# Kernel optimization log

Hardware: AMD Instinct MI355X
Metric: run time of the kernel (lower is better)

## Reference

```python
import jax, jax.numpy as jnp
import numpy as np

NUM_HEADS = 16

def _w8a8_linear(x_q, x_scale, w_q, w_scale, bias):
    # W8A8 GEMM with dynamic per-token input scale and per-output-channel weight scale
    # x_q: [N, Din] int8 values, w_q: [Dout, Din] int8 values
    acc = jnp.matmul(x_q.astype(jnp.float32), w_q.astype(jnp.float32).T)  # [N, Dout]
    return acc * (x_scale[:, None] * w_scale[None, :]) + bias[None, :]


def setup_inputs() -> dict:
    key = jax.random.key(0)
    ks = jax.random.split(key, 16)
    B, S, D = 2, 2048, 1024
    N = B * S
    def int8(k, shape):
        return jax.random.randint(k, shape, -127, 128, dtype=jnp.int32)
    inp = {
        "x_q": int8(ks[0], (N, D)),
        "x_scale": jax.random.uniform(ks[1], (N,), jnp.float32, 0.005, 0.02),
        "wq": int8(ks[2], (D, D)),
        "wq_scale": jax.random.uniform(ks[3], (D,), jnp.float32, 0.005, 0.02),
        "bq": jax.random.normal(ks[4], (D,), jnp.float32) * 0.02,
        "wk": int8(ks[5], (D, D)),
        "wk_scale": jax.random.uniform(ks[6], (D,), jnp.float32, 0.005, 0.02),
        "bk": jax.random.normal(ks[7], (D,), jnp.float32) * 0.02,
        "wv": int8(ks[8], (D, D)),
        "wv_scale": jax.random.uniform(ks[9], (D,), jnp.float32, 0.005, 0.02),
        "bv": jax.random.normal(ks[10], (D,), jnp.float32) * 0.02,
        "wo": int8(ks[11], (D, D)),
        "wo_scale": jax.random.uniform(ks[12], (D,), jnp.float32, 0.005, 0.02),
        "bo": jax.random.normal(ks[13], (D,), jnp.float32) * 0.02,
        "bsz": B,
        "qlen": S,
    }
    return inp


def reference(x_q, x_scale, wq, wq_scale, bq, wk, wk_scale, bk,
              wv, wv_scale, bv, wo, wo_scale, bo, bsz, qlen):
    D = wq.shape[0]
    hd = D // NUM_HEADS
    # quantized QKV projections (dequant fused into GEMM epilogue)
    q = _w8a8_linear(x_q, x_scale, wq, wq_scale, bq).reshape(bsz, qlen, NUM_HEADS, hd)
    k = _w8a8_linear(x_q, x_scale, wk, wk_scale, bk).reshape(bsz, qlen, NUM_HEADS, hd)
    v = _w8a8_linear(x_q, x_scale, wv, wv_scale, bv).reshape(bsz, qlen, NUM_HEADS, hd)
    # flash_attn_func(softmax_scale=None, causal=False) => scale = 1/sqrt(head_dim)
    scale = 1.0 / jnp.sqrt(jnp.float32(hd))
    scores = jnp.einsum('bqhd,bkhd->bhqk', q, k) * scale
    probs = jax.nn.softmax(scores, axis=-1)
    attn = jnp.einsum('bhqk,bkhd->bqhd', probs, v).reshape(bsz * qlen, D)
    # invoke_quant: dynamic per-token symmetric int8 quantization of attn output
    o_scale = jnp.max(jnp.abs(attn), axis=-1) / 127.0  # [N]
    o_q = jnp.clip(jnp.round(attn / o_scale[:, None]), -127.0, 127.0)
    # quantized out projection
    out = _w8a8_linear(o_q, o_scale, wo, wo_scale, bo)  # [N, D]
    return out
```

## Files before the change

kernel.cpp:

```cpp
#include <hip/hip_runtime.h>

#define D_MODEL 1024
#define NTOK    4096
#define SEQ     2048
#define NH      16
#define HD      64

typedef __bf16 bh8  __attribute__((ext_vector_type(8)));
typedef __bf16 bf4  __attribute__((ext_vector_type(4)));
typedef float  f32x4 __attribute__((ext_vector_type(4)));
typedef int    i32x4 __attribute__((ext_vector_type(4)));

__device__ __forceinline__ unsigned short f2bf(float f) {
  unsigned int u = __float_as_uint(f);
  u += 0x7fffu + ((u >> 16) & 1u);
  return (unsigned short)(u >> 16);
}
__device__ __forceinline__ float bf2f(unsigned short h) {
  return __uint_as_float(((unsigned int)h) << 16);
}
__device__ __forceinline__ float exp2a(float x) {
  float r; asm("v_exp_f32 %0, %1" : "=v"(r) : "v"(x)); return r;
}
__device__ __forceinline__ void gl16(const void* g, void* l) {
  __builtin_amdgcn_global_load_lds((const __attribute__((address_space(1))) unsigned int*)g,
                                   (__attribute__((address_space(3))) unsigned int*)l, 16, 0, 0);
}

__device__ __forceinline__ void pack_row(const int* src, unsigned* dst, int m, int t) {
  int4 w = *(const int4*)(src + (size_t)m * 1024 + t * 4);
  unsigned p01 = __builtin_amdgcn_perm((unsigned)w.y, (unsigned)w.x, 0x00000400u);
  unsigned p23 = __builtin_amdgcn_perm((unsigned)w.w, (unsigned)w.z, 0x00000400u);
  unsigned r   = __builtin_amdgcn_perm(p23, p01, 0x05040100u);
  int kg = t >> 4, c = (t >> 2) & 3, b4 = t & 3, sw = (m >> 1) & 3;
  dst[(size_t)m * 256 + kg * 16 + ((c ^ sw) << 2) + b4] = r;
}
__launch_bounds__(256)
__global__ void pack_x_k(const int* __restrict__ src, unsigned* __restrict__ dst) {
  pack_row(src, dst, blockIdx.x, threadIdx.x);
}
__launch_bounds__(256)
__global__ void pack_w_k(const int* __restrict__ s0, const int* __restrict__ s1,
                         const int* __restrict__ s2, const int* __restrict__ s3,
                         unsigned* __restrict__ d0, unsigned* __restrict__ d1,
                         unsigned* __restrict__ d2, unsigned* __restrict__ d3) {
  int wsel = blockIdx.x >> 10, m = blockIdx.x & 1023;
  const int* src = wsel == 0 ? s0 : wsel == 1 ? s1 : wsel == 2 ? s2 : s3;
  unsigned*  dst = wsel == 0 ? d0 : wsel == 1 ? d1 : wsel == 2 ? d2 : d3;
  pack_row(src, dst, m, threadIdx.x);
}

__launch_bounds__(256, 2)
__global__ void gemmQKV_k(const signed char* __restrict__ xp,
                          const signed char* __restrict__ wqp,
                          const signed char* __restrict__ wkp,
                          const signed char* __restrict__ wvp,
                          const float* __restrict__ xs,
                          const float* __restrict__ wqs, const float* __restrict__ bq,
                          const float* __restrict__ wks, const float* __restrict__ bk,
                          const float* __restrict__ wvs, const float* __restrict__ bv,
                          float SC,
                          unsigned short* __restrict__ qhi, unsigned short* __restrict__ qlo,
                          unsigned short* __restrict__ khi, unsigned short* __restrict__ klo,
                          unsigned short* __restrict__ vtw)
{
  __shared__ __align__(16) signed char As[2][8192];
  __shared__ __align__(16) signed char Bs[2][8192];
  const int id = blockIdx.x, z = id >> 8, rb = id & 255;
  const int t = threadIdx.x, wid = t >> 6, lane = t & 63, g = lane >> 4, li = lane & 15;
  const int wm = wid >> 1, wn = wid & 1;
  const signed char *Ap, *Bp;
  int m0, n0;
  if (z == 2) { Ap = wvp; Bp = xp; m0 = (rb & 7) * 128; n0 = (rb >> 3) * 128; }
  else        { Ap = xp; Bp = z ? wkp : wqp; m0 = (rb >> 3) * 128; n0 = (rb & 7) * 128; }

  i32x4 acc[4][4];
#pragma unroll
  for (int i = 0; i < 4; ++i)
#pragma unroll
    for (int j = 0; j < 4; ++j) acc[i][j] = (i32x4){0, 0, 0, 0};

  const int unitBase = wid * 2;
#pragma unroll
  for (int i = 0; i < 2; ++i) {
    int unit = (unitBase + i) * 64 + lane, r = unit >> 2, c = unit & 3;
    gl16(Ap + (size_t)(m0 + r) * 1024 + c * 16, (char*)As[0] + (unitBase + i) * 1024);
    gl16(Bp + (size_t)(n0 + r) * 1024 + c * 16, (char*)Bs[0] + (unitBase + i) * 1024);
  }
  __syncthreads();
  int p = 0;
#pragma unroll 1
  for (int ks = 0; ks < 16; ++ks) {
    if (ks < 15) {
      const int k0 = (ks + 1) * 64;
#pragma unroll
      for (int i = 0; i < 2; ++i) {
        int unit = (unitBase + i) * 64 + lane, r = unit >> 2, c = unit & 3;
        gl16(Ap + (size_t)(m0 + r) * 1024 + k0 + c * 16, (char*)As[p ^ 1] + (unitBase + i) * 1024);
        gl16(Bp + (size_t)(n0 + r) * 1024 + k0 + c * 16, (char*)Bs[p ^ 1] + (unitBase + i) * 1024);
      }
    }
    i32x4 af[4], bfr[4];
#pragma unroll
    for (int mt = 0; mt < 4; ++mt) {
      int row = wm * 64 + mt * 16 + li;
      af[mt] = *(const i32x4*)(As[p] + row * 64 + ((g ^ ((row >> 1) & 3)) << 4));
    }
#pragma unroll
    for (int nt = 0; nt < 4; ++nt) {
      int row = wn * 64 + nt * 16 + li;
      bfr[nt] = *(const i32x4*)(Bs[p] + row * 64 + ((g ^ ((row >> 1) & 3)) << 4));
    }
    __builtin_amdgcn_s_setprio(1);
#pragma unroll
    for (int mt = 0; mt < 4; ++mt)
#pragma unroll
      for (int nt = 0; nt < 4; ++nt)
        acc[mt][nt] = __builtin_amdgcn_mfma_i32_16x16x64_i8(af[mt], bfr[nt], acc[mt][nt], 0, 0, 0);
    __builtin_amdgcn_s_setprio(0);
    __syncthreads();
    p ^= 1;
  }

#pragma unroll
  for (int mt = 0; mt < 4; ++mt) {
#pragma unroll
    for (int nt = 0; nt < 4; ++nt) {
      const int nn = n0 + wn * 64 + nt * 16 + li;
#pragma unroll
      for (int r = 0; r < 4; ++r) {
        const int m = m0 + wm * 64 + mt * 16 + g * 4 + r;
        const float a = (float)acc[mt][nt][r];
        if (z == 2) {
          float f = a * (wvs[m] * xs[nn]) + bv[m];
          int hh = m >> 6, d = m & 63, bb = nn >> 11, s = nn & 2047;
          size_t o = (((size_t)(bb * NH + hh)) * HD + d) * SEQ + s;
          vtw[o] = f2bf(f);
        } else {
          const float* wsc = z ? wks : wqs;
          const float* wbi = z ? bk : bq;
          float f = (a * (xs[m] * wsc[nn]) + wbi[nn]) * (z ? 1.0f : SC);
          int bb = m >> 11, s = m & 2047, hh = nn >> 6, d = nn & 63;
          int dd = z ? ((((d >> 3) ^ (s & 7)) << 3) | (d & 7)) : d;
          size_t o = (((size_t)(bb * NH + hh)) * SEQ + s) * HD + dd;
          unsigned short hi = f2bf(f);
          unsigned short lo = f2bf(f - bf2f(hi));
          if (z) { khi[o] = hi; klo[o] = lo; }
          else   { qhi[o] = hi; qlo[o] = lo; }
        }
      }
    }
  }
}

__launch_bounds__(256, 2)
__global__ void gemmO_k(const signed char* __restrict__ Ap, const signed char* __restrict__ Bp,
                        const float* __restrict__ sA, const float* __restrict__ sB,
                        const float* __restrict__ bias, float* __restrict__ outF)
{
  __shared__ __align__(16) signed char As[2][8192];
  __shared__ __align__(16) signed char Bs[2][4096];
  const int id = blockIdx.x;
  const int m0 = (id >> 4) * 128, n0 = (id & 15) * 64;
  const int t = threadIdx.x, wid = t >> 6, lane = t & 63, g = lane >> 4, li = lane & 15;
  const int wm = wid >> 1, wn = wid & 1;

  i32x4 acc[4][2];
#pragma unroll
  for (int i = 0; i < 4; ++i)
#pragma unroll
    for (int j = 0; j < 2; ++j) acc[i][j] = (i32x4){0, 0, 0, 0};

#pragma unroll
  for (int i = 0; i < 2; ++i) {
    int unit = (wid * 2 + i) * 64 + lane, r = unit >> 2, c = unit & 3;
    gl16(Ap + (size_t)(m0 + r) * 1024 + c * 16, (char*)As[0] + (wid * 2 + i) * 1024);
  }
  { int unit = wid * 64 + lane, r = unit >> 2, c = unit & 3;
    gl16(Bp + (size_t)(n0 + r) * 1024 + c * 16, (char*)Bs[0] + wid * 1024); }
  __syncthreads();
  int p = 0;
#pragma unroll 1
  for (int ks = 0; ks < 16; ++ks) {
    if (ks < 15) {
      const int k0 = (ks + 1) * 64;
#pragma unroll
      for (int i = 0; i < 2; ++i) {
        int unit = (wid * 2 + i) * 64 + lane, r = unit >> 2, c = unit & 3;
        gl16(Ap + (size_t)(m0 + r) * 1024 + k0 + c * 16, (char*)As[p ^ 1] + (wid * 2 + i) * 1024);
      }
      { int unit = wid * 64 + lane, r = unit >> 2, c = unit & 3;
        gl16(Bp + (size_t)(n0 + r) * 1024 + k0 + c * 16, (char*)Bs[p ^ 1] + wid * 1024); }
    }
    i32x4 af[4], bfr[2];
#pragma unroll
    for (int mt = 0; mt < 4; ++mt) {
      int row = wm * 64 + mt * 16 + li;
      af[mt] = *(const i32x4*)(As[p] + row * 64 + ((g ^ ((row >> 1) & 3)) << 4));
    }
#pragma unroll
    for (int nt = 0; nt < 2; ++nt) {
      int row = wn * 32 + nt * 16 + li;
      bfr[nt] = *(const i32x4*)(Bs[p] + row * 64 + ((g ^ ((row >> 1) & 3)) << 4));
    }
    __builtin_amdgcn_s_setprio(1);
#pragma unroll
    for (int mt = 0; mt < 4; ++mt)
#pragma unroll
      for (int nt = 0; nt < 2; ++nt)
        acc[mt][nt] = __builtin_amdgcn_mfma_i32_16x16x64_i8(af[mt], bfr[nt], acc[mt][nt], 0, 0, 0);
    __builtin_amdgcn_s_setprio(0);
    __syncthreads();
    p ^= 1;
  }

#pragma unroll
  for (int mt = 0; mt < 4; ++mt)
#pragma unroll
    for (int nt = 0; nt < 2; ++nt) {
      const int nn = n0 + wn * 32 + nt * 16 + li;
#pragma unroll
      for (int r = 0; r < 4; ++r) {
        const int m = m0 + wm * 64 + mt * 16 + g * 4 + r;
        outF[(size_t)m * 1024 + nn] = (float)acc[mt][nt][r] * (sA[m] * sB[nn]) + bias[nn];
      }
    }
}

__launch_bounds__(256, 2)
__global__ void attn_k(const unsigned short* __restrict__ qhi, const unsigned short* __restrict__ qlo,
                       const unsigned short* __restrict__ khi, const unsigned short* __restrict__ klo,
                       const unsigned short* __restrict__ vt, float* __restrict__ attn)
{
  __shared__ __align__(16) unsigned short khs[2][4096], kls[2][4096];
  __shared__ __align__(16) unsigned short ps[4][2][1024];
  const int t = threadIdx.x;
  const int w = t >> 6, lane = t & 63, g = lane >> 4, li = lane & 15;
  const int q0 = blockIdx.x * 128, h = blockIdx.y, b = blockIdx.z;
  const int bh = b * NH + h;
  const int qA = q0 + w * 32 + li, qB = qA + 16;

  bh8 qhf[2][2], qlf[2][2];
#pragma unroll
  for (int kc = 0; kc < 2; ++kc) {
    qhf[0][kc] = *(const bh8*)(qhi + ((size_t)bh * SEQ + qA) * HD + kc * 32 + g * 8);
    qlf[0][kc] = *(const bh8*)(qlo + ((size_t)bh * SEQ + qA) * HD + kc * 32 + g * 8);
    qhf[1][kc] = *(const bh8*)(qhi + ((size_t)bh * SEQ + qB) * HD + kc * 32 + g * 8);
    qlf[1][kc] = *(const bh8*)(qlo + ((size_t)bh * SEQ + qB) * HD + kc * 32 + g * 8);
  }
  const unsigned short* kb = khi + (size_t)bh * SEQ * HD;
  const unsigned short* lb = klo + (size_t)bh * SEQ * HD;
  const unsigned short* vb = vt  + (size_t)bh * HD * SEQ;

  float m_run[2] = {-INFINITY, -INFINITY}, l_run[2] = {0.0f, 0.0f};
  f32x4 ot[2][4];
#pragma unroll
  for (int s = 0; s < 2; ++s)
#pragma unroll
    for (int i = 0; i < 4; ++i) ot[s][i] = (f32x4)0.0f;

#pragma unroll
  for (int i = 0; i < 2; ++i) {
    int unit = (w * 2 + i) * 64 + lane, r = unit >> 3, c = unit & 7;
    gl16(kb + (size_t)r * 64 + c * 8, (char*)khs[0] + (w * 2 + i) * 1024);
    gl16(lb + (size_t)r * 64 + c * 8, (char*)kls[0] + (w * 2 + i) * 1024);
  }

#pragma unroll 1
  for (int it = 0; it < 32; ++it) {
    const int kk0 = it * 64, cur = it & 1;
    __syncthreads();
    bh8 vreg[2][4];
#pragma unroll
    for (int kc2 = 0; kc2 < 2; ++kc2)
#pragma unroll
      for (int dt = 0; dt < 4; ++dt)
        vreg[kc2][dt] = *(const bh8*)(vb + (size_t)(dt * 16 + li) * SEQ + kk0 + kc2 * 32 + g * 8);
    if (it < 31) {
#pragma unroll
      for (int i = 0; i < 2; ++i) {
        int unit = (w * 2 + i) * 64 + lane, r = unit >> 3, c = unit & 7;
        gl16(kb + (size_t)(kk0 + 64 + r) * 64 + c * 8, (char*)khs[cur ^ 1] + (w * 2 + i) * 1024);
        gl16(lb + (size_t)(kk0 + 64 + r) * 64 + c * 8, (char*)kls[cur ^ 1] + (w * 2 + i) * 1024);
      }
    }
    f32x4 sa[2][4];
#pragma unroll
    for (int s = 0; s < 2; ++s)
#pragma unroll
      for (int i = 0; i < 4; ++i) sa[s][i] = (f32x4)0.0f;
#pragma unroll
    for (int kt2 = 0; kt2 < 4; ++kt2) {
      int row = kt2 * 16 + li, rx = row & 7;
#pragma unroll
      for (int kc = 0; kc < 2; ++kc) {
        bh8 kh = *(const bh8*)((const char*)khs[cur] + row * 128 + ((((kc << 2) | g) ^ rx) << 4));
        bh8 kl = *(const bh8*)((const char*)kls[cur] + row * 128 + ((((kc << 2) | g) ^ rx) << 4));
        __builtin_amdgcn_s_setprio(1);
        sa[0][kt2] = __builtin_amdgcn_mfma_f32_16x16x32_bf16(kh, qhf[0][kc], sa[0][kt2], 0, 0, 0);
        sa[1][kt2] = __builtin_amdgcn_mfma_f32_16x16x32_bf16(kh, qhf[1][kc], sa[1][kt2], 0, 0, 0);
        sa[0][kt2] = __builtin_amdgcn_mfma_f32_16x16x32_bf16(kh, qlf[0][kc], sa[0][kt2], 0, 0, 0);
        sa[1][kt2] = __builtin_amdgcn_mfma_f32_16x16x32_bf16(kh, qlf[1][kc], sa[1][kt2], 0, 0, 0);
        sa[0][kt2] = __builtin_amdgcn_mfma_f32_16x16x32_bf16(kl, qhf[0][kc], sa[0][kt2], 0, 0, 0);
        sa[1][kt2] = __builtin_amdgcn_mfma_f32_16x16x32_bf16(kl, qhf[1][kc], sa[1][kt2], 0, 0, 0);
        __builtin_amdgcn_s_setprio(0);
      }
    }
#pragma unroll
    for (int s = 0; s < 2; ++s) {
      float sm = -INFINITY;
#pragma unroll
      for (int kt2 = 0; kt2 < 4; ++kt2)
#pragma unroll
        for (int r = 0; r < 4; ++r) sm = fmaxf(sm, sa[s][kt2][r]);
      sm = fmaxf(sm, __shfl_xor(sm, 16));
      sm = fmaxf(sm, __shfl_xor(sm, 32));
      if (__any(sm > m_run[s] + 11.0f)) {
        float mn = fmaxf(m_run[s], sm);
        float alpha = exp2a(m_run[s] - mn);
        l_run[s] *= alpha;
#pragma unroll
        for (int i = 0; i < 4; ++i) ot[s][i] *= alpha;
        m_run[s] = mn;
      }
      float ts = 0.0f;
#pragma unroll
      for (int kt2 = 0; kt2 < 4; ++kt2)
#pragma unroll
        for (int r = 0; r < 4; ++r) {
          float e = exp2a(sa[s][kt2][r] - m_run[s]);
          sa[s][kt2][r] = e; ts += e;
        }
      ts += __shfl_xor(ts, 16);
      ts += __shfl_xor(ts, 32);
      l_run[s] += ts;
#pragma unroll
      for (int kt2 = 0; kt2 < 4; ++kt2) {
        bf4 pk = { (__bf16)sa[s][kt2][0], (__bf16)sa[s][kt2][1],
                   (__bf16)sa[s][kt2][2], (__bf16)sa[s][kt2][3] };
        int lchunk = (kt2 << 1) | (g >> 1);
        *(bf4*)((char*)ps[w][s] + li * 128 + ((lchunk ^ (li & 7)) << 4) + ((g & 1) << 3)) = pk;
      }
    }
    asm volatile("s_waitcnt lgkmcnt(0)" ::: "memory");
    __builtin_amdgcn_sched_barrier(0);
    bh8 pf[2][2];
#pragma unroll
    for (int s = 0; s < 2; ++s)
#pragma unroll
      for (int kc2 = 0; kc2 < 2; ++kc2)
        pf[s][kc2] = *(const bh8*)((const char*)ps[w][s] + li * 128 + ((((kc2 << 2) | g) ^ (li & 7)) << 4));
#pragma unroll
    for (int kc2 = 0; kc2 < 2; ++kc2) {
      __builtin_amdgcn_s_setprio(1);
#pragma unroll
      for (int dt = 0; dt < 4; ++dt) {
        ot[0][dt] = __builtin_amdgcn_mfma_f32_16x16x32_bf16(vreg[kc2][dt], pf[0][kc2], ot[0][dt], 0, 0, 0);
        ot[1][dt] = __builtin_amdgcn_mfma_f32_16x16x32_bf16(vreg[kc2][dt], pf[1][kc2], ot[1][dt], 0, 0, 0);
      }
      __builtin_amdgcn_s_setprio(0);
    }
  }

#pragma unroll
  for (int s = 0; s < 2; ++s) {
    const float inv = 1.0f / l_run[s];
    const int n = b * SEQ + (s ? qB : qA);
#pragma unroll
    for (int dt = 0; dt < 4; ++dt) {
      float4 o4;
      o4.x = ot[s][dt][0] * inv; o4.y = ot[s][dt][1] * inv;
      o4.z = ot[s][dt][2] * inv; o4.w = ot[s][dt][3] * inv;
      *(float4*)(attn + (size_t)n * D_MODEL + h * HD + dt * 16 + g * 4) = o4;
    }
  }
}

__launch_bounds__(256)
__global__ void quant_k(const float* __restrict__ attn, unsigned* __restrict__ oqp,
                        float* __restrict__ osc)
{
  const int row = blockIdx.x, t = threadIdx.x;
  float4 v = *(const float4*)(attn + (size_t)row * D_MODEL + t * 4);
  float mx = fmaxf(fmaxf(fabsf(v.x), fabsf(v.y)), fmaxf(fabsf(v.z), fabsf(v.w)));
#pragma unroll
  for (int off = 1; off < 64; off <<= 1) mx = fmaxf(mx, __shfl_xor(mx, off));
  __shared__ float red[4];
  if ((t & 63) == 0) red[t >> 6] = mx;
  __syncthreads();
  mx = fmaxf(fmaxf(red[0], red[1]), fmaxf(red[2], red[3]));
  const float s = mx / 127.0f;
  if (t == 0) osc[row] = s;
  int q0 = (int)fminf(fmaxf(rintf(v.x / s), -127.f), 127.f);
  int q1 = (int)fminf(fmaxf(rintf(v.y / s), -127.f), 127.f);
  int q2 = (int)fminf(fmaxf(rintf(v.z / s), -127.f), 127.f);
  int q3 = (int)fminf(fmaxf(rintf(v.w / s), -127.f), 127.f);
  unsigned pk = ((unsigned)q0 & 255u) | (((unsigned)q1 & 255u) << 8) |
                (((unsigned)q2 & 255u) << 16) | (((unsigned)q3 & 255u) << 24);
  int kg = t >> 4, c = (t >> 2) & 3, b4 = t & 3, sw = (row >> 1) & 3;
  oqp[(size_t)row * 256 + kg * 16 + ((c ^ sw) << 2) + b4] = pk;
}

extern "C" void kernel_launch(void* const* d_in, const int* in_sizes, int n_in,
                              void* d_out, int out_size, void* d_ws, size_t ws_size,
                              hipStream_t stream)
{
  const int*   x   = (const int*)d_in[0];
  const float* xs  = (const float*)d_in[1];
  const int*   wq  = (const int*)d_in[2];
  const float* wqs = (const float*)d_in[3];
  const float* bq  = (const float*)d_in[4];
  const int*   wk  = (const int*)d_in[5];
  const float* wks = (const float*)d_in[6];
  const float* bk  = (const float*)d_in[7];
  const int*   wv  = (const int*)d_in[8];
  const float* wvs = (const float*)d_in[9];
  const float* bv  = (const float*)d_in[10];
  const int*   wo  = (const int*)d_in[11];
  const float* wos = (const float*)d_in[12];
  const float* bo  = (const float*)d_in[13];
  float* out = (float*)d_out;

  char* ws = (char*)d_ws;
  const size_t MB = 1024 * 1024;
  unsigned* xp  = (unsigned*)(ws);
  unsigned* wqp = (unsigned*)(ws + 4 * MB);
  unsigned* wkp = (unsigned*)(ws + 5 * MB);
  unsigned* wvp = (unsigned*)(ws + 6 * MB);
  unsigned* wop = (unsigned*)(ws + 7 * MB);
  unsigned short* qhi = (unsigned short*)(ws + 8 * MB);
  unsigned short* qlo = (unsigned short*)(ws + 16 * MB);
  unsigned short* khi = (unsigned short*)(ws + 24 * MB);
  unsigned short* klo = (unsigned short*)(ws + 32 * MB);
  unsigned short* vtw = (unsigned short*)(ws + 40 * MB);
  float*          att = (float*)(ws + 48 * MB);
  unsigned*       oqp = (unsigned*)(ws);
  float*          osc = (float*)(ws + 4 * MB);

  const float SC = 0.125f * 1.44269504088896340736f;
  dim3 blk(256);
  pack_x_k<<<dim3(4096), blk, 0, stream>>>(x, xp);
  pack_w_k<<<dim3(4096), blk, 0, stream>>>(wq, wk, wv, wo, wqp, wkp, wvp, wop);
  gemmQKV_k<<<dim3(768), blk, 0, stream>>>((const signed char*)xp, (const signed char*)wqp,
                                           (const signed char*)wkp, (const signed char*)wvp,
                                           xs, wqs, bq, wks, bk, wvs, bv, SC,
                                           qhi, qlo, khi, klo, vtw);
  attn_k<<<dim3(16, NH, 2), blk, 0, stream>>>(qhi, qlo, khi, klo, vtw, att);
  quant_k<<<dim3(4096), blk, 0, stream>>>(att, oqp, osc);
  gemmO_k<<<dim3(512), blk, 0, stream>>>((const signed char*)oqp, (const signed char*)wop,
                                         osc, wos, bo, out);
}
```

Baseline: 258.4 us.

## Shrink QKV GEMM tiles, reshape warp layout, and load attention K directly from global

The QKV GEMM moves from 128x128 to 128x64 tiles, doubling the grid, and each warp now covers 32 rows across the full 64 columns. The output GEMM gets the same warp-layout change. The attention kernel drops the LDS double-buffered K staging and its swizzle and reads K hi/lo fragments straight from global memory into registers each iteration. The aim is more parallelism and fewer barriers and LDS traffic, at the cost of less operand reuse in the GEMM and uncoalesced, unprefetched global loads for K in attention.

```diff
diff --git a/kernel.cpp b/kernel.cpp
--- a/kernel.cpp
+++ b/kernel.cpp
@@ -65,28 +65,27 @@
                           unsigned short* __restrict__ vtw)
 {
   __shared__ __align__(16) signed char As[2][8192];
-  __shared__ __align__(16) signed char Bs[2][8192];
-  const int id = blockIdx.x, z = id >> 8, rb = id & 255;
+  __shared__ __align__(16) signed char Bs[2][4096];
+  const int id = blockIdx.x, z = id >> 9, rb = id & 511;
   const int t = threadIdx.x, wid = t >> 6, lane = t & 63, g = lane >> 4, li = lane & 15;
-  const int wm = wid >> 1, wn = wid & 1;
   const signed char *Ap, *Bp;
   int m0, n0;
-  if (z == 2) { Ap = wvp; Bp = xp; m0 = (rb & 7) * 128; n0 = (rb >> 3) * 128; }
-  else        { Ap = xp; Bp = z ? wkp : wqp; m0 = (rb >> 3) * 128; n0 = (rb & 7) * 128; }
-
-  i32x4 acc[4][4];
-#pragma unroll
-  for (int i = 0; i < 4; ++i)
+  if (z == 2) { Ap = wvp; Bp = xp; m0 = (rb >> 6) * 128; n0 = (rb & 63) * 64; }
+  else        { Ap = xp; Bp = z ? wkp : wqp; m0 = (rb >> 4) * 128; n0 = (rb & 15) * 64; }
+
+  i32x4 acc[2][4];
+#pragma unroll
+  for (int i = 0; i < 2; ++i)
 #pragma unroll
     for (int j = 0; j < 4; ++j) acc[i][j] = (i32x4){0, 0, 0, 0};
 
-  const int unitBase = wid * 2;
 #pragma unroll
   for (int i = 0; i < 2; ++i) {
-    int unit = (unitBase + i) * 64 + lane, r = unit >> 2, c = unit & 3;
-    gl16(Ap + (size_t)(m0 + r) * 1024 + c * 16, (char*)As[0] + (unitBase + i) * 1024);
-    gl16(Bp + (size_t)(n0 + r) * 1024 + c * 16, (char*)Bs[0] + (unitBase + i) * 1024);
-  }
+    int unit = (wid * 2 + i) * 64 + lane, r = unit >> 2, c = unit & 3;
+    gl16(Ap + (size_t)(m0 + r) * 1024 + c * 16, (char*)As[0] + (wid * 2 + i) * 1024);
+  }
+  { int unit = wid * 64 + lane, r = unit >> 2, c = unit & 3;
+    gl16(Bp + (size_t)(n0 + r) * 1024 + c * 16, (char*)Bs[0] + wid * 1024); }
   __syncthreads();
   int p = 0;
 #pragma unroll 1
@@ -95,25 +94,26 @@
       const int k0 = (ks + 1) * 64;
 #pragma unroll
       for (int i = 0; i < 2; ++i) {
-        int unit = (unitBase + i) * 64 + lane, r = unit >> 2, c = unit & 3;
-        gl16(Ap + (size_t)(m0 + r) * 1024 + k0 + c * 16, (char*)As[p ^ 1] + (unitBase + i) * 1024);
-        gl16(Bp + (size_t)(n0 + r) * 1024 + k0 + c * 16, (char*)Bs[p ^ 1] + (unitBase + i) * 1024);
-      }
-    }
-    i32x4 af[4], bfr[4];
-#pragma unroll
-    for (int mt = 0; mt < 4; ++mt) {
-      int row = wm * 64 + mt * 16 + li;
+        int unit = (wid * 2 + i) * 64 + lane, r = unit >> 2, c = unit & 3;
+        gl16(Ap + (size_t)(m0 + r) * 1024 + k0 + c * 16, (char*)As[p ^ 1] + (wid * 2 + i) * 1024);
+      }
+      { int unit = wid * 64 + lane, r = unit >> 2, c = unit & 3;
+        gl16(Bp + (size_t)(n0 + r) * 1024 + k0 + c * 16, (char*)Bs[p ^ 1] + wid * 1024); }
+    }
+    i32x4 af[2], bfr[4];
+#pragma unroll
+    for (int mt = 0; mt < 2; ++mt) {
+      int row = wid * 32 + mt * 16 + li;
       af[mt] = *(const i32x4*)(As[p] + row * 64 + ((g ^ ((row >> 1) & 3)) << 4));
     }
 #pragma unroll
     for (int nt = 0; nt < 4; ++nt) {
-      int row = wn * 64 + nt * 16 + li;
+      int row = nt * 16 + li;
       bfr[nt] = *(const i32x4*)(Bs[p] + row * 64 + ((g ^ ((row >> 1) & 3)) << 4));
     }
     __builtin_amdgcn_s_setprio(1);
 #pragma unroll
-    for (int mt = 0; mt < 4; ++mt)
+    for (int mt = 0; mt < 2; ++mt)
 #pragma unroll
       for (int nt = 0; nt < 4; ++nt)
         acc[mt][nt] = __builtin_amdgcn_mfma_i32_16x16x64_i8(af[mt], bfr[nt], acc[mt][nt], 0, 0, 0);
@@ -123,26 +123,24 @@
   }
 
 #pragma unroll
-  for (int mt = 0; mt < 4; ++mt) {
+  for (int mt = 0; mt < 2; ++mt) {
 #pragma unroll
     for (int nt = 0; nt < 4; ++nt) {
-      const int nn = n0 + wn * 64 + nt * 16 + li;
+      const int nn = n0 + nt * 16 + li;
 #pragma unroll
       for (int r = 0; r < 4; ++r) {
-        const int m = m0 + wm * 64 + mt * 16 + g * 4 + r;
+        const int m = m0 + wid * 32 + mt * 16 + g * 4 + r;
         const float a = (float)acc[mt][nt][r];
         if (z == 2) {
           float f = a * (wvs[m] * xs[nn]) + bv[m];
           int hh = m >> 6, d = m & 63, bb = nn >> 11, s = nn & 2047;
-          size_t o = (((size_t)(bb * NH + hh)) * HD + d) * SEQ + s;
-          vtw[o] = f2bf(f);
+          vtw[(((size_t)(bb * NH + hh)) * HD + d) * SEQ + s] = f2bf(f);
         } else {
           const float* wsc = z ? wks : wqs;
           const float* wbi = z ? bk : bq;
           float f = (a * (xs[m] * wsc[nn]) + wbi[nn]) * (z ? 1.0f : SC);
           int bb = m >> 11, s = m & 2047, hh = nn >> 6, d = nn & 63;
-          int dd = z ? ((((d >> 3) ^ (s & 7)) << 3) | (d & 7)) : d;
-          size_t o = (((size_t)(bb * NH + hh)) * SEQ + s) * HD + dd;
+          size_t o = (((size_t)(bb * NH + hh)) * SEQ + s) * HD + d;
           unsigned short hi = f2bf(f);
           unsigned short lo = f2bf(f - bf2f(hi));
           if (z) { khi[o] = hi; klo[o] = lo; }
@@ -163,13 +161,12 @@
   const int id = blockIdx.x;
   const int m0 = (id >> 4) * 128, n0 = (id & 15) * 64;
   const int t = threadIdx.x, wid = t >> 6, lane = t & 63, g = lane >> 4, li = lane & 15;
-  const int wm = wid >> 1, wn = wid & 1;
-
-  i32x4 acc[4][2];
-#pragma unroll
-  for (int i = 0; i < 4; ++i)
-#pragma unroll
-    for (int j = 0; j < 2; ++j) acc[i][j] = (i32x4){0, 0, 0, 0};
+
+  i32x4 acc[2][4];
+#pragma unroll
+  for (int i = 0; i < 2; ++i)
+#pragma unroll
+    for (int j = 0; j < 4; ++j) acc[i][j] = (i32x4){0, 0, 0, 0};
 
 #pragma unroll
   for (int i = 0; i < 2; ++i) {
@@ -192,22 +189,22 @@
       { int unit = wid * 64 + lane, r = unit >> 2, c = unit & 3;
         gl16(Bp + (size_t)(n0 + r) * 1024 + k0 + c * 16, (char*)Bs[p ^ 1] + wid * 1024); }
     }
-    i32x4 af[4], bfr[2];
-#pragma unroll
-    for (int mt = 0; mt < 4; ++mt) {
-      int row = wm * 64 + mt * 16 + li;
+    i32x4 af[2], bfr[4];
+#pragma unroll
+    for (int mt = 0; mt < 2; ++mt) {
+      int row = wid * 32 + mt * 16 + li;
       af[mt] = *(const i32x4*)(As[p] + row * 64 + ((g ^ ((row >> 1) & 3)) << 4));
     }
 #pragma unroll
-    for (int nt = 0; nt < 2; ++nt) {
-      int row = wn * 32 + nt * 16 + li;
+    for (int nt = 0; nt < 4; ++nt) {
+      int row = nt * 16 + li;
       bfr[nt] = *(const i32x4*)(Bs[p] + row * 64 + ((g ^ ((row >> 1) & 3)) << 4));
     }
     __builtin_amdgcn_s_setprio(1);
 #pragma unroll
-    for (int mt = 0; mt < 4; ++mt)
-#pragma unroll
-      for (int nt = 0; nt < 2; ++nt)
+    for (int mt = 0; mt < 2; ++mt)
+#pragma unroll
+      for (int nt = 0; nt < 4; ++nt)
         acc[mt][nt] = __builtin_amdgcn_mfma_i32_16x16x64_i8(af[mt], bfr[nt], acc[mt][nt], 0, 0, 0);
     __builtin_amdgcn_s_setprio(0);
     __syncthreads();
@@ -215,13 +212,13 @@
   }
 
 #pragma unroll
-  for (int mt = 0; mt < 4; ++mt)
-#pragma unroll
-    for (int nt = 0; nt < 2; ++nt) {
-      const int nn = n0 + wn * 32 + nt * 16 + li;
+  for (int mt = 0; mt < 2; ++mt)
+#pragma unroll
+    for (int nt = 0; nt < 4; ++nt) {
+      const int nn = n0 + nt * 16 + li;
 #pragma unroll
       for (int r = 0; r < 4; ++r) {
-        const int m = m0 + wm * 64 + mt * 16 + g * 4 + r;
+        const int m = m0 + wid * 32 + mt * 16 + g * 4 + r;
         outF[(size_t)m * 1024 + nn] = (float)acc[mt][nt][r] * (sA[m] * sB[nn]) + bias[nn];
       }
     }
@@ -232,7 +229,6 @@
                        const unsigned short* __restrict__ khi, const unsigned short* __restrict__ klo,
                        const unsigned short* __restrict__ vt, float* __restrict__ attn)
 {
-  __shared__ __align__(16) unsigned short khs[2][4096], kls[2][4096];
   __shared__ __align__(16) unsigned short ps[4][2][1024];
   const int t = threadIdx.x;
   const int w = t >> 6, lane = t & 63, g = lane >> 4, li = lane & 15;
@@ -259,53 +255,42 @@
 #pragma unroll
     for (int i = 0; i < 4; ++i) ot[s][i] = (f32x4)0.0f;
 
-#pragma unroll
-  for (int i = 0; i < 2; ++i) {
-    int unit = (w * 2 + i) * 64 + lane, r = unit >> 3, c = unit & 7;
-    gl16(kb + (size_t)r * 64 + c * 8, (char*)khs[0] + (w * 2 + i) * 1024);
-    gl16(lb + (size_t)r * 64 + c * 8, (char*)kls[0] + (w * 2 + i) * 1024);
-  }
-
 #pragma unroll 1
   for (int it = 0; it < 32; ++it) {
-    const int kk0 = it * 64, cur = it & 1;
-    __syncthreads();
-    bh8 vreg[2][4];
+    const int kk0 = it * 64;
+    bh8 kh[4][2], kl[4][2];
+#pragma unroll
+    for (int kt2 = 0; kt2 < 4; ++kt2)
+#pragma unroll
+      for (int kc = 0; kc < 2; ++kc) {
+        kh[kt2][kc] = *(const bh8*)(kb + (size_t)(kk0 + kt2 * 16 + li) * HD + kc * 32 + g * 8);
+        kl[kt2][kc] = *(const bh8*)(lb + (size_t)(kk0 + kt2 * 16 + li) * HD + kc * 32 + g * 8);
+      }
+    f32x4 sa[2][4];
+#pragma unroll
+    for (int s = 0; s < 2; ++s)
+#pragma unroll
+      for (int i = 0; i < 4; ++i) sa[s][i] = (f32x4)0.0f;
+#pragma unroll
+    for (int kt2 = 0; kt2 < 4; ++kt2) {
+#pragma unroll
+      for (int kc = 0; kc < 2; ++kc) {
+        __builtin_amdgcn_s_setprio(1);
+        sa[0][kt2] = __builtin_amdgcn_mfma_f32_16x16x32_bf16(kh[kt2][kc], qhf[0][kc], sa[0][kt2], 0, 0, 0);
+        sa[1][kt2] = __builtin_amdgcn_mfma_f32_16x16x32_bf16(kh[kt2][kc], qhf[1][kc], sa[1][kt2], 0, 0, 0);
+        sa[0][kt2] = __builtin_amdgcn_mfma_f32_16x16x32_bf16(kh[kt2][kc], qlf[0][kc], sa[0][kt2], 0, 0, 0);
+        sa[1][kt2] = __builtin_amdgcn_mfma_f32_16x16x32_bf16(kh[kt2][kc], qlf[1][kc], sa[1][kt2], 0, 0, 0);
+        sa[0][kt2] = __builtin_amdgcn_mfma_f32_16x16x32_bf16(kl[kt2][kc], qhf[0][kc], sa[0][kt2], 0, 0, 0);
+        sa[1][kt2] = __builtin_amdgcn_mfma_f32_16x16x32_bf16(kl[kt2][kc], qhf[1][kc], sa[1][kt2], 0, 0, 0);
+        __builtin_amdgcn_s_setprio(0);
+      }
+    }
+    bh8 vv[2][4];
 #pragma unroll
     for (int kc2 = 0; kc2 < 2; ++kc2)
 #pragma unroll
       for (int dt = 0; dt < 4; ++dt)
-        vreg[kc2][dt] = *(const bh8*)(vb + (size_t)(dt * 16 + li) * SEQ + kk0 + kc2 * 32 + g * 8);
-    if (it < 31) {
-#pragma unroll
-      for (int i = 0; i < 2; ++i) {
-        int unit = (w * 2 + i) * 64 + lane, r = unit >> 3, c = unit & 7;
-        gl16(kb + (size_t)(kk0 + 64 + r) * 64 + c * 8, (char*)khs[cur ^ 1] + (w * 2 + i) * 1024);
-        gl16(lb + (size_t)(kk0 + 64 + r) * 64 + c * 8, (char*)kls[cur ^ 1] + (w * 2 + i) * 1024);
-      }
-    }
-    f32x4 sa[2][4];
-#pragma unroll
-    for (int s = 0; s < 2; ++s)
-#pragma unroll
-      for (int i = 0; i < 4; ++i) sa[s][i] = (f32x4)0.0f;
-#pragma unroll
-    for (int kt2 = 0; kt2 < 4; ++kt2) {
-      int row = kt2 * 16 + li, rx = row & 7;
-#pragma unroll
-      for (int kc = 0; kc < 2; ++kc) {
-        bh8 kh = *(const bh8*)((const char*)khs[cur] + row * 128 + ((((kc << 2) | g) ^ rx) << 4));
-        bh8 kl = *(const bh8*)((const char*)kls[cur] + row * 128 + ((((kc << 2) | g) ^ rx) << 4));
-        __builtin_amdgcn_s_setprio(1);
-        sa[0][kt2] = __builtin_amdgcn_mfma_f32_16x16x32_bf16(kh, qhf[0][kc], sa[0][kt2], 0, 0, 0);
-        sa[1][kt2] = __builtin_amdgcn_mfma_f32_16x16x32_bf16(kh, qhf[1][kc], sa[1][kt2], 0, 0, 0);
-        sa[0][kt2] = __builtin_amdgcn_mfma_f32_16x16x32_bf16(kh, qlf[0][kc], sa[0][kt2], 0, 0, 0);
-        sa[1][kt2] = __builtin_amdgcn_mfma_f32_16x16x32_bf16(kh, qlf[1][kc], sa[1][kt2], 0, 0, 0);
-        sa[0][kt2] = __builtin_amdgcn_mfma_f32_16x16x32_bf16(kl, qhf[0][kc], sa[0][kt2], 0, 0, 0);
-        sa[1][kt2] = __builtin_amdgcn_mfma_f32_16x16x32_bf16(kl, qhf[1][kc], sa[1][kt2], 0, 0, 0);
-        __builtin_amdgcn_s_setprio(0);
-      }
-    }
+        vv[kc2][dt] = *(const bh8*)(vb + (size_t)(dt * 16 + li) * SEQ + kk0 + kc2 * 32 + g * 8);
 #pragma unroll
     for (int s = 0; s < 2; ++s) {
       float sm = -INFINITY;
@@ -355,8 +340,8 @@
       __builtin_amdgcn_s_setprio(1);
 #pragma unroll
       for (int dt = 0; dt < 4; ++dt) {
-        ot[0][dt] = __builtin_amdgcn_mfma_f32_16x16x32_bf16(vreg[kc2][dt], pf[0][kc2], ot[0][dt], 0, 0, 0);
-        ot[1][dt] = __builtin_amdgcn_mfma_f32_16x16x32_bf16(vreg[kc2][dt], pf[1][kc2], ot[1][dt], 0, 0, 0);
+        ot[0][dt] = __builtin_amdgcn_mfma_f32_16x16x32_bf16(vv[kc2][dt], pf[0][kc2], ot[0][dt], 0, 0, 0);
+        ot[1][dt] = __builtin_amdgcn_mfma_f32_16x16x32_bf16(vv[kc2][dt], pf[1][kc2], ot[1][dt], 0, 0, 0);
       }
       __builtin_amdgcn_s_setprio(0);
     }
@@ -441,10 +426,10 @@
   dim3 blk(256);
   pack_x_k<<<dim3(4096), blk, 0, stream>>>(x, xp);
   pack_w_k<<<dim3(4096), blk, 0, stream>>>(wq, wk, wv, wo, wqp, wkp, wvp, wop);
-  gemmQKV_k<<<dim3(768), blk, 0, stream>>>((const signed char*)xp, (const signed char*)wqp,
-                                           (const signed char*)wkp, (const signed char*)wvp,
-                                           xs, wqs, bq, wks, bk, wvs, bv, SC,
-                                           qhi, qlo, khi, klo, vtw);
+  gemmQKV_k<<<dim3(1536), blk, 0, stream>>>((const signed char*)xp, (const signed char*)wqp,
+                                            (const signed char*)wkp, (const signed char*)wvp,
+                                            xs, wqs, bq, wks, bk, wvs, bv, SC,
+                                            qhi, qlo, khi, klo, vtw);
   attn_k<<<dim3(16, NH, 2), blk, 0, stream>>>(qhi, qlo, khi, klo, vtw, att);
   quant_k<<<dim3(4096), blk, 0, stream>>>(att, oqp, osc);
   gemmO_k<<<dim3(512), blk, 0, stream>>>((const signed char*)oqp, (const signed char*)wop,
```

After: 333.5 us. 29.0% more time.
